# Kernel optimization log

Measured on AMD Instinct MI355X. Metric: run time of the kernel, lower is better.

Reference implementation:

```python
import jax, jax.numpy as jnp
import numpy as np


def setup_inputs() -> dict:
    key = jax.random.key(0)
    ks = jax.random.split(key, 5)
    B, H, S, C, Dh = 2, 16, 2048, 2048, 64
    HID = H * Dh
    return {
        "q": jax.random.normal(ks[0], (B, H, S, Dh), dtype=jnp.float32),
        "k": jax.random.normal(ks[1], (B, H, C + S, Dh), dtype=jnp.float32),
        "v": jax.random.normal(ks[2], (B, H, C + S, Dh), dtype=jnp.float32),
        "memory_length": 256,
        "W": jax.random.normal(ks[3], (HID, HID), dtype=jnp.float32) / np.sqrt(HID),
        "b": jax.random.normal(ks[4], (HID,), dtype=jnp.float32) * 0.01,
    }


def _build_mask(S, KV, memory_length):
    # KV = CACHE_LEN + S; columns >= CACHE_LEN + memory_length are restricted.
    C = KV - S
    rows = jnp.arange(S)[:, None]          # query position in [0, S)
    cols = jnp.arange(KV)[None, :]         # key position in [0, KV)
    restricted = cols >= (C + memory_length)
    # memory rows (< memory_length) never see restricted cols;
    # other rows: strictly-upper-triangular masking (col - (C+mem) > row - mem)
    mem_row = rows < memory_length
    future = (cols - (C + memory_length)) > (rows - memory_length)
    return (restricted & (mem_row | future))  # bool [S, KV], True = masked


def reference(q, k, v, memory_length, W, b):
    B, H, S, Dh = q.shape
    KV = k.shape[2]
    HID = H * Dh
    scale = 1.0 / np.sqrt(Dh).astype(np.float32)
    scores = jnp.einsum('bhsd,bhtd->bhst', q, k) * scale   # [B,H,S,KV]
    mask2d = _build_mask(S, KV, memory_length)             # [S,KV] bool
    scores = jnp.where(mask2d[None, None], -jnp.inf, scores)
    attn_w = jax.nn.softmax(scores, axis=-1)
    attn = jnp.einsum('bhst,bhtd->bshd', attn_w, v).reshape(B, S, HID)
    out = attn @ W.T + b
    # torch module returns full [B,H,S,KV] float mask of 0/1
    mask_full = jnp.broadcast_to(mask2d.astype(q.dtype), (B, H, S, KV))
    return out, mask_full
```

## Files before the change

kernel.cpp:

```cpp
#include <hip/hip_runtime.h>
#include <hip/hip_bf16.h>
#include <math.h>

typedef __bf16 bf16;
typedef __bf16 bf16x4 __attribute__((ext_vector_type(4)));
typedef __bf16 bf16x8 __attribute__((ext_vector_type(8)));
typedef float f32x4 __attribute__((ext_vector_type(4)));

#define MFMA(a, b, c) __builtin_amdgcn_mfma_f32_16x16x32_bf16((a), (b), (c), 0, 0, 0)

constexpr int Bb  = 2;
constexpr int Hh  = 16;
constexpr int Ss  = 2048;
constexpr int KVv = 4096;
constexpr int Dd  = 64;
constexpr int Cc  = KVv - Ss;
constexpr int HID = Hh * Dd;

constexpr float QSCL = 0.125f * 1.44269504088896340736f;

constexpr size_t MASK_F4   = (size_t)Bb * Hh * Ss * KVv / 4;
constexpr size_t SCR_BYTES = 16777216ull + 16777216ull + 2097152ull + 8388608ull;
constexpr size_t M2_F4     = MASK_F4 - (2097152ull + 8388608ull) / 16;
constexpr size_t M1_F4     = 44000000;

__device__ __forceinline__ void write_mask_range(
    float* __restrict__ mout, int mem, size_t lo, size_t hi,
    int mblk, int nmblk, int tid, int nthr)
{
    const int R = Cc + mem;
    const size_t stride = (size_t)nmblk * nthr;
    for (size_t i = lo + (size_t)mblk * nthr + tid; i < hi; i += stride) {
        size_t flat = i * 4;
        int t = (int)(flat & (size_t)(KVv - 1));
        int s = (int)((flat >> 12) & (size_t)(Ss - 1));
        int thr = (s < mem) ? R : (s + Cc + 1);
        f32x4 vv;
        vv[0] = (float)(t >= thr);
        vv[1] = (float)(t + 1 >= thr);
        vv[2] = (float)(t + 2 >= thr);
        vv[3] = (float)(t + 3 >= thr);
        __builtin_nontemporal_store(vv, (f32x4*)(mout + flat));
    }
}

__global__ __launch_bounds__(256) void prep_kernel(
    const float* __restrict__ K, const float* __restrict__ W,
    const float* __restrict__ V,
    bf16* __restrict__ Kb, bf16* __restrict__ Wb, bf16* __restrict__ Vt)
{
    const int bid = blockIdx.x;
    if (bid < 2048) {
        __shared__ __align__(16) bf16 T[64][72];
        const int bh = bid >> 6;
        const int t0 = (bid & 63) * 64;
        const int row = threadIdx.x >> 2;
        const int cg  = threadIdx.x & 3;
        const float* vb = V + (size_t)bh * KVv * Dd + (size_t)(t0 + row) * Dd + cg * 16;
        float4 x0 = ((const float4*)vb)[0];
        float4 x1 = ((const float4*)vb)[1];
        float4 x2 = ((const float4*)vb)[2];
        float4 x3 = ((const float4*)vb)[3];
        float xs[16] = {x0.x,x0.y,x0.z,x0.w, x1.x,x1.y,x1.z,x1.w,
                        x2.x,x2.y,x2.z,x2.w, x3.x,x3.y,x3.z,x3.w};
#pragma unroll
        for (int j = 0; j < 16; ++j)
            T[cg * 16 + j][row] = (bf16)xs[j];
        __syncthreads();
        const int d = row;
        bf16* o = Vt + (size_t)bh * Dd * KVv + (size_t)d * KVv + t0 + cg * 16;
        ((bf16x8*)o)[0] = *(const bf16x8*)&T[d][cg * 16];
        ((bf16x8*)o)[1] = *(const bf16x8*)&T[d][cg * 16 + 8];
        return;
    }
    const size_t nK4 = (size_t)Bb * Hh * KVv * Dd / 4;
    const size_t nW4 = (size_t)HID * HID / 4;
    const size_t total = nK4 + nW4;
    const size_t stride = (size_t)(gridDim.x - 2048) * 256;
    for (size_t i = (size_t)(bid - 2048) * 256 + threadIdx.x; i < total; i += stride) {
        float4 x = (i < nK4) ? ((const float4*)K)[i] : ((const float4*)W)[i - nK4];
        bf16x4 t;
        t[0] = (bf16)x.x; t[1] = (bf16)x.y; t[2] = (bf16)x.z; t[3] = (bf16)x.w;
        if (i < nK4) ((bf16x4*)Kb)[i] = t;
        else         ((bf16x4*)Wb)[i - nK4] = t;
    }
}

template <bool MASKED>
__device__ __forceinline__ void kv_tile(
    int t0, const bf16* __restrict__ kb_p, const bf16* __restrict__ vt_p,
    const bf16x8 qa[2], const int thr[4], int tid, int lr, int lg,
    bf16 (*__restrict__ Klds)[72], bf16 (*__restrict__ Vlds)[72],
    bf16 (*__restrict__ Pw)[72], f32x4 acco[4], float lsum[4])
{
    {
        const int row = tid >> 3, c8 = tid & 7;
        bf16x8 kx = *(const bf16x8*)(kb_p + (size_t)(t0 + row) * Dd + c8 * 8);
        bf16x8 vx = *(const bf16x8*)(vt_p + (size_t)row * KVv + t0 + c8 * 8);
        *(bf16x8*)&Klds[row][c8 * 8] = kx;
        *(bf16x8*)&Vlds[row][c8 * 8] = vx;
    }
    __syncthreads();

    f32x4 accs[4];
#pragma unroll
    for (int kg = 0; kg < 4; ++kg) accs[kg] = (f32x4){0.f, 0.f, 0.f, 0.f};
    __builtin_amdgcn_s_setprio(1);
#pragma unroll
    for (int ks = 0; ks < 2; ++ks) {
#pragma unroll
        for (int kg = 0; kg < 4; ++kg) {
            bf16x8 kf = *(const bf16x8*)&Klds[kg * 16 + lr][ks * 32 + lg * 8];
            accs[kg] = MFMA(qa[ks], kf, accs[kg]);
        }
    }
    __builtin_amdgcn_s_setprio(0);

#pragma unroll
    for (int r = 0; r < 4; ++r) {
#pragma unroll
        for (int kg = 0; kg < 4; ++kg) {
            float sl = accs[kg][r];
            if (MASKED) {
                int tcol = t0 + kg * 16 + lr;
                sl = (tcol < thr[r]) ? sl : -1e30f;
            }
            accs[kg][r] = __builtin_amdgcn_exp2f(sl);
        }
        lsum[r] += (accs[0][r] + accs[1][r]) + (accs[2][r] + accs[3][r]);
#pragma unroll
        for (int kg = 0; kg < 4; ++kg)
            Pw[lg * 4 + r][kg * 16 + lr] = (bf16)accs[kg][r];
    }
    asm volatile("s_waitcnt lgkmcnt(0)" ::: "memory");

    __builtin_amdgcn_s_setprio(1);
#pragma unroll
    for (int ks = 0; ks < 2; ++ks) {
        bf16x8 pa = *(const bf16x8*)&Pw[lr][ks * 32 + lg * 8];
#pragma unroll
        for (int dg = 0; dg < 4; ++dg) {
            bf16x8 vf = *(const bf16x8*)&Vlds[dg * 16 + lr][ks * 32 + lg * 8];
            acco[dg] = MFMA(pa, vf, acco[dg]);
        }
    }
    __builtin_amdgcn_s_setprio(0);
    __syncthreads();
}

__global__ __launch_bounds__(512) void fused_attn_kernel(
    const float* __restrict__ q, const bf16* __restrict__ Kb,
    const bf16* __restrict__ Vtb, const int* __restrict__ memp,
    bf16* __restrict__ attnb, float* __restrict__ mout)
{
    __shared__ __align__(16) bf16 Klds[64][72];
    __shared__ __align__(16) bf16 Vlds[64][72];
    __shared__ __align__(16) bf16 Plds[8][16][72];

    const int fid = blockIdx.x;
    const int mem = *memp;
    if (fid >= 512) {
        write_mask_range(mout, mem, 0, M1_F4, fid - 512, gridDim.x - 512,
                         threadIdx.x, 512);
        return;
    }
    const int xcd = fid & 7;
    const int slot = fid >> 3;
    const int qblk = slot & 15;
    const int bh = (slot >> 4) * 8 + xcd;

    const int tid = threadIdx.x;
    const int w  = tid >> 6;
    const int l  = tid & 63;
    const int lr = l & 15;
    const int lg = l >> 4;
    const int q0 = qblk * 128;
    const int R = Cc + mem;

    const float* qp   = q   + (size_t)bh * Ss * Dd;
    const bf16*  kb_p = Kb  + (size_t)bh * KVv * Dd;
    const bf16*  vt_p = Vtb + (size_t)bh * Dd * KVv;

    const int qrow = q0 + w * 16 + lr;
    bf16x8 qa[2];
#pragma unroll
    for (int ks = 0; ks < 2; ++ks) {
        const float* p8 = qp + (size_t)qrow * Dd + ks * 32 + lg * 8;
        float4 x0 = *(const float4*)p8;
        float4 x1 = *(const float4*)(p8 + 4);
        bf16x8 a;
        a[0] = (bf16)(x0.x * QSCL); a[1] = (bf16)(x0.y * QSCL);
        a[2] = (bf16)(x0.z * QSCL); a[3] = (bf16)(x0.w * QSCL);
        a[4] = (bf16)(x1.x * QSCL); a[5] = (bf16)(x1.y * QSCL);
        a[6] = (bf16)(x1.z * QSCL); a[7] = (bf16)(x1.w * QSCL);
        qa[ks] = a;
    }

    int thr[4];
#pragma unroll
    for (int r = 0; r < 4; ++r) {
        int qabs = q0 + w * 16 + lg * 4 + r;
        thr[r] = (qabs < mem) ? R : (qabs + Cc + 1);
    }
    const int qmaxb = q0 + 127;
    int kv_end = (qmaxb < mem) ? R : (qmaxb + Cc + 1);
    if (kv_end > KVv) kv_end = KVv;
    int thr_min = (q0 < mem) ? R : (q0 + Cc + 1);
    int p1_end = thr_min & ~63;
    if (p1_end > kv_end) p1_end = kv_end;

    f32x4 acco[4];
#pragma unroll
    for (int dg = 0; dg < 4; ++dg) acco[dg] = (f32x4){0.f, 0.f, 0.f, 0.f};
    float lsum[4] = {0.f, 0.f, 0.f, 0.f};

    for (int t0 = 0; t0 < p1_end; t0 += 64)
        kv_tile<false>(t0, kb_p, vt_p, qa, thr, tid, lr, lg, Klds, Vlds, Plds[w], acco, lsum);
    for (int t0 = p1_end; t0 < kv_end; t0 += 64)
        kv_tile<true>(t0, kb_p, vt_p, qa, thr, tid, lr, lg, Klds, Vlds, Plds[w], acco, lsum);

    const int b = bh >> 4, h = bh & 15;
#pragma unroll
    for (int r = 0; r < 4; ++r) {
        float s = lsum[r];
        s += __shfl_xor(s, 1);
        s += __shfl_xor(s, 2);
        s += __shfl_xor(s, 4);
        s += __shfl_xor(s, 8);
        float inv = 1.f / s;
        int qabs = q0 + w * 16 + lg * 4 + r;
        bf16* dst = attnb + (size_t)(b * Ss + qabs) * HID + h * Dd;
#pragma unroll
        for (int dg = 0; dg < 4; ++dg)
            dst[dg * 16 + lr] = (bf16)(acco[dg][r] * inv);
    }
}

__global__ __launch_bounds__(256) void fused_proj_kernel(
    const bf16* __restrict__ A, const bf16* __restrict__ Wb,
    const float* __restrict__ bias, float* __restrict__ out,
    const int* __restrict__ memp, float* __restrict__ mout, size_t mhi)
{
    __shared__ __align__(16) bf16 Alds[64][72];
    __shared__ __align__(16) bf16 Wlds[64][72];

    const int fid = blockIdx.x;
    if (fid >= 1024) {
        write_mask_range(mout, *memp, M1_F4, mhi, fid - 1024, gridDim.x - 1024,
                         threadIdx.x, 256);
        return;
    }
    const int xcd = fid & 7;
    const int slot = fid >> 3;
    const int o0 = ((slot & 1) * 8 + xcd) * 64;
    const int i0 = (slot >> 1) * 64;

    const int tid = threadIdx.x;
    const int w  = tid >> 6;
    const int l  = tid & 63;
    const int lr = l & 15;
    const int lg = l >> 4;

    f32x4 acc[4];
#pragma unroll
    for (int og = 0; og < 4; ++og) acc[og] = (f32x4){0.f, 0.f, 0.f, 0.f};

    for (int kc = 0; kc < HID; kc += 64) {
        const int row = tid >> 2, cg = tid & 3;
        bf16x8 a0 = ((const bf16x8*)(A  + (size_t)(i0 + row) * HID + kc + cg * 16))[0];
        bf16x8 a1 = ((const bf16x8*)(A  + (size_t)(i0 + row) * HID + kc + cg * 16))[1];
        bf16x8 w0 = ((const bf16x8*)(Wb + (size_t)(o0 + row) * HID + kc + cg * 16))[0];
        bf16x8 w1 = ((const bf16x8*)(Wb + (size_t)(o0 + row) * HID + kc + cg * 16))[1];
        *(bf16x8*)&Alds[row][cg * 16]     = a0;
        *(bf16x8*)&Alds[row][cg * 16 + 8] = a1;
        *(bf16x8*)&Wlds[row][cg * 16]     = w0;
        *(bf16x8*)&Wlds[row][cg * 16 + 8] = w1;
        __syncthreads();
        __builtin_amdgcn_s_setprio(1);
#pragma unroll
        for (int ks = 0; ks < 2; ++ks) {
            bf16x8 af = *(const bf16x8*)&Alds[w * 16 + lr][ks * 32 + lg * 8];
#pragma unroll
            for (int og = 0; og < 4; ++og) {
                bf16x8 wf = *(const bf16x8*)&Wlds[og * 16 + lr][ks * 32 + lg * 8];
                acc[og] = MFMA(af, wf, acc[og]);
            }
        }
        __builtin_amdgcn_s_setprio(0);
        __syncthreads();
    }

#pragma unroll
    for (int r = 0; r < 4; ++r) {
        int i = i0 + w * 16 + lg * 4 + r;
#pragma unroll
        for (int og = 0; og < 4; ++og) {
            int o = o0 + og * 16 + lr;
            __builtin_nontemporal_store(acc[og][r] + bias[o], &out[(size_t)i * HID + o]);
        }
    }
}

__global__ __launch_bounds__(256) void mask_tail_kernel(
    float* __restrict__ mout, const int* __restrict__ memp)
{
    write_mask_range(mout, *memp, M2_F4, MASK_F4, blockIdx.x, gridDim.x,
                     threadIdx.x, 256);
}

extern "C" void kernel_launch(void* const* d_in, const int* in_sizes, int n_in,
                              void* d_out, int out_size, void* d_ws, size_t ws_size,
                              hipStream_t stream)
{
    (void)in_sizes; (void)n_in; (void)out_size;
    const float* q    = (const float*)d_in[0];
    const float* k    = (const float*)d_in[1];
    const float* v    = (const float*)d_in[2];
    const int*   memp = (const int*)d_in[3];
    const float* W    = (const float*)d_in[4];
    const float* bias = (const float*)d_in[5];

    float* out     = (float*)d_out;
    float* maskout = out + (size_t)Bb * Ss * HID;

    const bool use_ws = ws_size >= SCR_BYTES;
    char* scr = use_ws ? (char*)d_ws
                       : (char*)maskout + MASK_F4 * 16 - SCR_BYTES;
    bf16* Kbf   = (bf16*)scr;
    bf16* Vtb   = Kbf + (size_t)Bb * Hh * KVv * Dd;
    bf16* Wbf   = Vtb + (size_t)Bb * Hh * KVv * Dd;
    bf16* attnb = Wbf + (size_t)HID * HID;

    const size_t mhi = use_ws ? MASK_F4 : M2_F4;

    prep_kernel<<<dim3(2048 + 1024), 256, 0, stream>>>(k, W, v, Kbf, Wbf, Vtb);
    fused_attn_kernel<<<dim3(512 + 1024), 512, 0, stream>>>(q, Kbf, Vtb, memp, attnb, maskout);
    fused_proj_kernel<<<dim3(1024 + 512), 256, 0, stream>>>(attnb, Wbf, bias, out, memp, maskout, mhi);
    if (!use_ws)
        mask_tail_kernel<<<dim3(256), 256, 0, stream>>>(maskout, memp);
}
```

Baseline: 268.4 us.

## Fuse K/V/W bf16 conversion into attention and projection loads, drop prep kernel

Removes the separate prep kernel that converted K, W to bf16 and transposed V. The conversion now happens inside the attention and projection tile loads: K is converted per tile, V is transposed into LDS from fp32, and W is converted in the GEMM load. This drops one launch and the write and re-read of the bf16 scratch copies. In exchange each query block re-reads fp32 K/V, doubling global read bytes per tile and adding conversion ALU work on the critical path. The mask writer also emits two float4 stores per thread, and the tail kernel grid is halved.

```diff
diff --git a/kernel.cpp b/kernel.cpp
--- a/kernel.cpp
+++ b/kernel.cpp
@@ -19,86 +19,73 @@
 
 constexpr float QSCL = 0.125f * 1.44269504088896340736f;
 
-constexpr size_t MASK_F4   = (size_t)Bb * Hh * Ss * KVv / 4;
-constexpr size_t SCR_BYTES = 16777216ull + 16777216ull + 2097152ull + 8388608ull;
-constexpr size_t M2_F4     = MASK_F4 - (2097152ull + 8388608ull) / 16;
-constexpr size_t M1_F4     = 44000000;
+constexpr size_t MASK_F4     = (size_t)Bb * Hh * Ss * KVv / 4;
+constexpr size_t ATTNB_BYTES = (size_t)Bb * Ss * HID * 2;
+constexpr size_t M1_F4       = 44000000;
+constexpr size_t M2_F4       = MASK_F4 - ATTNB_BYTES / 16;
 
 __device__ __forceinline__ void write_mask_range(
-    float* __restrict__ mout, int mem, size_t lo, size_t hi,
+    float* __restrict__ mout, int mem, size_t lo4, size_t hi4,
     int mblk, int nmblk, int tid, int nthr)
 {
     const int R = Cc + mem;
+    const size_t lo = lo4 >> 1, hi = hi4 >> 1;
     const size_t stride = (size_t)nmblk * nthr;
-    for (size_t i = lo + (size_t)mblk * nthr + tid; i < hi; i += stride) {
-        size_t flat = i * 4;
+    for (size_t p = lo + (size_t)mblk * nthr + tid; p < hi; p += stride) {
+        size_t flat = p * 8;
         int t = (int)(flat & (size_t)(KVv - 1));
         int s = (int)((flat >> 12) & (size_t)(Ss - 1));
         int thr = (s < mem) ? R : (s + Cc + 1);
-        f32x4 vv;
-        vv[0] = (float)(t >= thr);
-        vv[1] = (float)(t + 1 >= thr);
-        vv[2] = (float)(t + 2 >= thr);
-        vv[3] = (float)(t + 3 >= thr);
-        __builtin_nontemporal_store(vv, (f32x4*)(mout + flat));
-    }
-}
-
-__global__ __launch_bounds__(256) void prep_kernel(
-    const float* __restrict__ K, const float* __restrict__ W,
-    const float* __restrict__ V,
-    bf16* __restrict__ Kb, bf16* __restrict__ Wb, bf16* __restrict__ Vt)
-{
-    const int bid = blockIdx.x;
-    if (bid < 2048) {
-        __shared__ __align__(16) bf16 T[64][72];
-        const int bh = bid >> 6;
-        const int t0 = (bid & 63) * 64;
-        const int row = threadIdx.x >> 2;
-        const int cg  = threadIdx.x & 3;
-        const float* vb = V + (size_t)bh * KVv * Dd + (size_t)(t0 + row) * Dd + cg * 16;
-        float4 x0 = ((const float4*)vb)[0];
-        float4 x1 = ((const float4*)vb)[1];
-        float4 x2 = ((const float4*)vb)[2];
-        float4 x3 = ((const float4*)vb)[3];
-        float xs[16] = {x0.x,x0.y,x0.z,x0.w, x1.x,x1.y,x1.z,x1.w,
-                        x2.x,x2.y,x2.z,x2.w, x3.x,x3.y,x3.z,x3.w};
-#pragma unroll
-        for (int j = 0; j < 16; ++j)
-            T[cg * 16 + j][row] = (bf16)xs[j];
-        __syncthreads();
-        const int d = row;
-        bf16* o = Vt + (size_t)bh * Dd * KVv + (size_t)d * KVv + t0 + cg * 16;
-        ((bf16x8*)o)[0] = *(const bf16x8*)&T[d][cg * 16];
-        ((bf16x8*)o)[1] = *(const bf16x8*)&T[d][cg * 16 + 8];
-        return;
-    }
-    const size_t nK4 = (size_t)Bb * Hh * KVv * Dd / 4;
-    const size_t nW4 = (size_t)HID * HID / 4;
-    const size_t total = nK4 + nW4;
-    const size_t stride = (size_t)(gridDim.x - 2048) * 256;
-    for (size_t i = (size_t)(bid - 2048) * 256 + threadIdx.x; i < total; i += stride) {
-        float4 x = (i < nK4) ? ((const float4*)K)[i] : ((const float4*)W)[i - nK4];
-        bf16x4 t;
-        t[0] = (bf16)x.x; t[1] = (bf16)x.y; t[2] = (bf16)x.z; t[3] = (bf16)x.w;
-        if (i < nK4) ((bf16x4*)Kb)[i] = t;
-        else         ((bf16x4*)Wb)[i - nK4] = t;
+        f32x4 v0, v1;
+        v0[0] = (float)(t     >= thr); v0[1] = (float)(t + 1 >= thr);
+        v0[2] = (float)(t + 2 >= thr); v0[3] = (float)(t + 3 >= thr);
+        v1[0] = (float)(t + 4 >= thr); v1[1] = (float)(t + 5 >= thr);
+        v1[2] = (float)(t + 6 >= thr); v1[3] = (float)(t + 7 >= thr);
+        __builtin_nontemporal_store(v0, (f32x4*)(mout + flat));
+        __builtin_nontemporal_store(v1, (f32x4*)(mout + flat + 4));
     }
 }
 
 template <bool MASKED>
 __device__ __forceinline__ void kv_tile(
-    int t0, const bf16* __restrict__ kb_p, const bf16* __restrict__ vt_p,
+    int t0, const float* __restrict__ kfp, const float* __restrict__ vfp,
     const bf16x8 qa[2], const int thr[4], int tid, int lr, int lg,
     bf16 (*__restrict__ Klds)[72], bf16 (*__restrict__ Vlds)[72],
     bf16 (*__restrict__ Pw)[72], f32x4 acco[4], float lsum[4])
 {
-    {
-        const int row = tid >> 3, c8 = tid & 7;
-        bf16x8 kx = *(const bf16x8*)(kb_p + (size_t)(t0 + row) * Dd + c8 * 8);
-        bf16x8 vx = *(const bf16x8*)(vt_p + (size_t)row * KVv + t0 + c8 * 8);
-        *(bf16x8*)&Klds[row][c8 * 8] = kx;
-        *(bf16x8*)&Vlds[row][c8 * 8] = vx;
+    if (tid < 256) {
+        const int row = tid >> 2, c16 = (tid & 3) * 16;
+        const float* kp4 = kfp + (size_t)(t0 + row) * Dd + c16;
+        float4 k0 = ((const float4*)kp4)[0];
+        float4 k1 = ((const float4*)kp4)[1];
+        float4 k2 = ((const float4*)kp4)[2];
+        float4 k3 = ((const float4*)kp4)[3];
+        bf16x8 lo, hi;
+        lo[0] = (bf16)k0.x; lo[1] = (bf16)k0.y; lo[2] = (bf16)k0.z; lo[3] = (bf16)k0.w;
+        lo[4] = (bf16)k1.x; lo[5] = (bf16)k1.y; lo[6] = (bf16)k1.z; lo[7] = (bf16)k1.w;
+        hi[0] = (bf16)k2.x; hi[1] = (bf16)k2.y; hi[2] = (bf16)k2.z; hi[3] = (bf16)k2.w;
+        hi[4] = (bf16)k3.x; hi[5] = (bf16)k3.y; hi[6] = (bf16)k3.z; hi[7] = (bf16)k3.w;
+        *(bf16x8*)&Klds[row][c16]     = lo;
+        *(bf16x8*)&Klds[row][c16 + 8] = hi;
+    } else {
+        const int t2 = tid - 256;
+        const int r4 = (t2 & 15) * 4, c4 = (t2 >> 4) * 4;
+        const float* vb = vfp + (size_t)(t0 + r4) * Dd + c4;
+        float4 a0 = *(const float4*)(vb);
+        float4 a1 = *(const float4*)(vb + Dd);
+        float4 a2 = *(const float4*)(vb + 2 * Dd);
+        float4 a3 = *(const float4*)(vb + 3 * Dd);
+        const float* f0 = (const float*)&a0;
+        const float* f1 = (const float*)&a1;
+        const float* f2 = (const float*)&a2;
+        const float* f3 = (const float*)&a3;
+#pragma unroll
+        for (int i = 0; i < 4; ++i) {
+            bf16x4 t;
+            t[0] = (bf16)f0[i]; t[1] = (bf16)f1[i];
+            t[2] = (bf16)f2[i]; t[3] = (bf16)f3[i];
+            *(bf16x4*)&Vlds[c4 + i][r4] = t;
+        }
     }
     __syncthreads();
 
@@ -149,8 +136,8 @@
 }
 
 __global__ __launch_bounds__(512) void fused_attn_kernel(
-    const float* __restrict__ q, const bf16* __restrict__ Kb,
-    const bf16* __restrict__ Vtb, const int* __restrict__ memp,
+    const float* __restrict__ q, const float* __restrict__ k,
+    const float* __restrict__ v, const int* __restrict__ memp,
     bf16* __restrict__ attnb, float* __restrict__ mout)
 {
     __shared__ __align__(16) bf16 Klds[64][72];
@@ -177,9 +164,9 @@
     const int q0 = qblk * 128;
     const int R = Cc + mem;
 
-    const float* qp   = q   + (size_t)bh * Ss * Dd;
-    const bf16*  kb_p = Kb  + (size_t)bh * KVv * Dd;
-    const bf16*  vt_p = Vtb + (size_t)bh * Dd * KVv;
+    const float* qp  = q + (size_t)bh * Ss * Dd;
+    const float* kfp = k + (size_t)bh * KVv * Dd;
+    const float* vfp = v + (size_t)bh * KVv * Dd;
 
     const int qrow = q0 + w * 16 + lr;
     bf16x8 qa[2];
@@ -215,9 +202,9 @@
     float lsum[4] = {0.f, 0.f, 0.f, 0.f};
 
     for (int t0 = 0; t0 < p1_end; t0 += 64)
-        kv_tile<false>(t0, kb_p, vt_p, qa, thr, tid, lr, lg, Klds, Vlds, Plds[w], acco, lsum);
+        kv_tile<false>(t0, kfp, vfp, qa, thr, tid, lr, lg, Klds, Vlds, Plds[w], acco, lsum);
     for (int t0 = p1_end; t0 < kv_end; t0 += 64)
-        kv_tile<true>(t0, kb_p, vt_p, qa, thr, tid, lr, lg, Klds, Vlds, Plds[w], acco, lsum);
+        kv_tile<true>(t0, kfp, vfp, qa, thr, tid, lr, lg, Klds, Vlds, Plds[w], acco, lsum);
 
     const int b = bh >> 4, h = bh & 15;
 #pragma unroll
@@ -237,7 +224,7 @@
 }
 
 __global__ __launch_bounds__(256) void fused_proj_kernel(
-    const bf16* __restrict__ A, const bf16* __restrict__ Wb,
+    const bf16* __restrict__ A, const float* __restrict__ W,
     const float* __restrict__ bias, float* __restrict__ out,
     const int* __restrict__ memp, float* __restrict__ mout, size_t mhi)
 {
@@ -266,15 +253,24 @@
     for (int og = 0; og < 4; ++og) acc[og] = (f32x4){0.f, 0.f, 0.f, 0.f};
 
     for (int kc = 0; kc < HID; kc += 64) {
-        const int row = tid >> 2, cg = tid & 3;
-        bf16x8 a0 = ((const bf16x8*)(A  + (size_t)(i0 + row) * HID + kc + cg * 16))[0];
-        bf16x8 a1 = ((const bf16x8*)(A  + (size_t)(i0 + row) * HID + kc + cg * 16))[1];
-        bf16x8 w0 = ((const bf16x8*)(Wb + (size_t)(o0 + row) * HID + kc + cg * 16))[0];
-        bf16x8 w1 = ((const bf16x8*)(Wb + (size_t)(o0 + row) * HID + kc + cg * 16))[1];
-        *(bf16x8*)&Alds[row][cg * 16]     = a0;
-        *(bf16x8*)&Alds[row][cg * 16 + 8] = a1;
-        *(bf16x8*)&Wlds[row][cg * 16]     = w0;
-        *(bf16x8*)&Wlds[row][cg * 16 + 8] = w1;
+        const int row = tid >> 2, c16 = (tid & 3) * 16;
+        const bf16* ap = A + (size_t)(i0 + row) * HID + kc + c16;
+        bf16x8 a0 = ((const bf16x8*)ap)[0];
+        bf16x8 a1 = ((const bf16x8*)ap)[1];
+        const float* wp = W + (size_t)(o0 + row) * HID + kc + c16;
+        float4 w0 = ((const float4*)wp)[0];
+        float4 w1 = ((const float4*)wp)[1];
+        float4 w2 = ((const float4*)wp)[2];
+        float4 w3 = ((const float4*)wp)[3];
+        bf16x8 wlo, whi;
+        wlo[0] = (bf16)w0.x; wlo[1] = (bf16)w0.y; wlo[2] = (bf16)w0.z; wlo[3] = (bf16)w0.w;
+        wlo[4] = (bf16)w1.x; wlo[5] = (bf16)w1.y; wlo[6] = (bf16)w1.z; wlo[7] = (bf16)w1.w;
+        whi[0] = (bf16)w2.x; whi[1] = (bf16)w2.y; whi[2] = (bf16)w2.z; whi[3] = (bf16)w2.w;
+        whi[4] = (bf16)w3.x; whi[5] = (bf16)w3.y; whi[6] = (bf16)w3.z; whi[7] = (bf16)w3.w;
+        *(bf16x8*)&Alds[row][c16]     = a0;
+        *(bf16x8*)&Alds[row][c16 + 8] = a1;
+        *(bf16x8*)&Wlds[row][c16]     = wlo;
+        *(bf16x8*)&Wlds[row][c16 + 8] = whi;
         __syncthreads();
         __builtin_amdgcn_s_setprio(1);
 #pragma unroll
@@ -323,19 +319,14 @@
     float* out     = (float*)d_out;
     float* maskout = out + (size_t)Bb * Ss * HID;
 
-    const bool use_ws = ws_size >= SCR_BYTES;
-    char* scr = use_ws ? (char*)d_ws
-                       : (char*)maskout + MASK_F4 * 16 - SCR_BYTES;
-    bf16* Kbf   = (bf16*)scr;
-    bf16* Vtb   = Kbf + (size_t)Bb * Hh * KVv * Dd;
-    bf16* Wbf   = Vtb + (size_t)Bb * Hh * KVv * Dd;
-    bf16* attnb = Wbf + (size_t)HID * HID;
+    const bool use_ws = ws_size >= ATTNB_BYTES;
+    bf16* attnb = use_ws ? (bf16*)d_ws
+                         : (bf16*)((char*)maskout + M2_F4 * 16);
 
     const size_t mhi = use_ws ? MASK_F4 : M2_F4;
 
-    prep_kernel<<<dim3(2048 + 1024), 256, 0, stream>>>(k, W, v, Kbf, Wbf, Vtb);
-    fused_attn_kernel<<<dim3(512 + 1024), 512, 0, stream>>>(q, Kbf, Vtb, memp, attnb, maskout);
-    fused_proj_kernel<<<dim3(1024 + 512), 256, 0, stream>>>(attnb, Wbf, bias, out, memp, maskout, mhi);
+    fused_attn_kernel<<<dim3(512 + 1024), 512, 0, stream>>>(q, k, v, memp, attnb, maskout);
+    fused_proj_kernel<<<dim3(1024 + 512), 256, 0, stream>>>(attnb, W, bias, out, memp, maskout, mhi);
     if (!use_ws)
-        mask_tail_kernel<<<dim3(256), 256, 0, stream>>>(maskout, memp);
-}
+        mask_tail_kernel<<<dim3(128), 256, 0, stream>>>(maskout, memp);
+}
```

Measured after the change: 609.6 us. 2.27x slower.
